# Optimization experiments

Hardware: AMD Instinct MI355X
Metric: run time of the kernel (lower is better)

## Reference

```python
import jax, jax.numpy as jnp
import numpy as np
import math

DIM = 768
K1 = 112
K2 = 224


def setup_inputs() -> dict:
    key = jax.random.key(0)
    ks = jax.random.split(key, 10)
    B, N, D = 256, 196, DIM
    inp = {
        "rgb_patches": jax.random.normal(ks[0], (B, N, D), jnp.float32),
        "nir_patches": jax.random.normal(ks[1], (B, N, D), jnp.float32),
        "tir_patches": jax.random.normal(ks[2], (B, N, D), jnp.float32),
        "rgb_global": jax.random.normal(ks[3], (B, D), jnp.float32),
        "nir_global": jax.random.normal(ks[4], (B, D), jnp.float32),
        "tir_global": jax.random.normal(ks[5], (B, D), jnp.float32),
        # nn.Linear params (W_v is defined in the torch module but never used in forward)
        "Wq": jax.random.normal(ks[6], (D, D), jnp.float32) / math.sqrt(D),
        "bq": jnp.zeros((D,), jnp.float32),
        "Wk": jax.random.normal(ks[7], (D, D), jnp.float32) / math.sqrt(D),
        "bk": jnp.zeros((D,), jnp.float32),
    }
    return inp


def _scatter_ones(idx, B, n):
    # idx: [B, K] in [0, n] where value n means "drop" (scattered into pad slot)
    rows = jnp.arange(B)[:, None]
    m = jnp.zeros((B, n + 1), jnp.float32).at[rows, idx].set(1.0)
    return m[:, :n]


def _intra_mask(patches, g, scale):
    # scores over own-modality patches
    B, N, _ = patches.shape
    scores = jax.nn.softmax(jnp.einsum('bd,bnd->bn', g, patches) * scale, axis=1)
    _, idx = jax.lax.top_k(scores, min(K1, N))
    return _scatter_ones(idx, B, N)


def _split_scatter(idx, B, n_a, n_b):
    # idx indexes concat([a (len n_a), b (len n_b)]); route to two masks
    idx_a = jnp.where(idx < n_a, idx, n_a)          # pad slot n_a when not a
    idx_b = jnp.where(idx >= n_a, idx - n_a, n_b)   # pad slot n_b when not b
    return _scatter_ones(idx_a, B, n_a), _scatter_ones(idx_b, B, n_b)


def reference(rgb_patches, nir_patches, tir_patches, rgb_global, nir_global, tir_global, Wq, bq, Wk, bk):
    B, n_rgb, D = rgb_patches.shape
    n_nir = nir_patches.shape[1]
    n_tir = tir_patches.shape[1]
    scale = 1.0 / math.sqrt(D)

    # ---- intra-modal selection ----
    rgb_mask_i = _intra_mask(rgb_patches, rgb_global, scale)
    nir_mask_i = _intra_mask(nir_patches, nir_global, scale)
    tir_mask_i = _intra_mask(tir_patches, tir_global, scale)

    # ---- inter-modal selection ----
    queries = jnp.stack([rgb_global, nir_global, tir_global], axis=1)        # [B,3,D]
    keys = jnp.concatenate([rgb_patches, nir_patches, tir_patches], axis=1)  # [B,3N,D]
    q = queries @ Wq.T + bq
    k = keys @ Wk.T + bk
    scores = jax.nn.softmax(jnp.einsum('bqd,bnd->bqn', q, k) * scale, axis=2)

    rgb_scores = jnp.concatenate([scores[:, 0, n_rgb:n_rgb + n_nir], scores[:, 0, n_rgb + n_nir:]], axis=1)
    nir_scores = jnp.concatenate([scores[:, 1, :n_rgb], scores[:, 1, n_rgb + n_nir:]], axis=1)
    tir_scores = jnp.concatenate([scores[:, 2, :n_rgb], scores[:, 2, n_rgb:n_rgb + n_nir]], axis=1)

    _, rgb_idx = jax.lax.top_k(rgb_scores, min(K2, rgb_scores.shape[1]))
    _, nir_idx = jax.lax.top_k(nir_scores, min(K2, nir_scores.shape[1]))
    _, tir_idx = jax.lax.top_k(tir_scores, min(K2, tir_scores.shape[1]))

    # rgb query selects among [nir, tir]; nir query among [rgb, tir]; tir query among [rgb, nir]
    nir_m1, tir_m1 = _split_scatter(rgb_idx, B, n_nir, n_tir)
    rgb_m1, tir_m2 = _split_scatter(nir_idx, B, n_rgb, n_tir)
    rgb_m2, nir_m2 = _split_scatter(tir_idx, B, n_rgb, n_nir)

    rgb_mask_c = jnp.maximum(rgb_m1, rgb_m2)
    nir_mask_c = jnp.maximum(nir_m1, nir_m2)
    tir_mask_c = jnp.maximum(tir_m1, tir_m2)

    # ---- union of masks, apply ----
    rgb_mask = (rgb_mask_c + rgb_mask_i > 0).astype(rgb_patches.dtype)[..., None]
    nir_mask = (nir_mask_c + nir_mask_i > 0).astype(nir_patches.dtype)[..., None]
    tir_mask = (tir_mask_c + tir_mask_i > 0).astype(tir_patches.dtype)[..., None]

    return (rgb_patches * rgb_mask, nir_patches * nir_mask, tir_patches * tir_mask)
```

## Files before the change

### kernel.cpp

```cpp
#include <hip/hip_runtime.h>

#define DD   768
#define BB   256
#define NN   196
#define KK1  112
#define KK2  224
#define RTOT (BB*3)
#define CAND (2*NN)


__global__ __launch_bounds__(256) void gemm_q(
    const float* __restrict__ g0, const float* __restrict__ g1,
    const float* __restrict__ g2, const float* __restrict__ Wq,
    const float* __restrict__ bq, double* __restrict__ Qh)
{
    __shared__ float As[32][33];
    __shared__ float Ws[32][33];
    const int t  = threadIdx.x;
    const int tx = t & 15, ty = t >> 4;
    const int i0 = blockIdx.y * 32, j0 = blockIdx.x * 32;
    double a00 = 0, a01 = 0, a10 = 0, a11 = 0;
    for (int kk = 0; kk < DD; kk += 32) {
        for (int s = 0; s < 4; ++s) {
            int idx = t + s * 256;
            int r = idx >> 5, c = idx & 31;
            int row = i0 + r;
            int b = row / 3, q = row - b * 3;
            const float* gp = (q == 0) ? g0 : (q == 1) ? g1 : g2;
            As[r][c] = gp[b * DD + kk + c];
            Ws[r][c] = Wq[(j0 + r) * DD + kk + c];
        }
        __syncthreads();
        for (int k = 0; k < 32; ++k) {
            double x0 = (double)As[ty][k],      x1 = (double)As[ty + 16][k];
            double y0 = (double)Ws[tx][k],      y1 = (double)Ws[tx + 16][k];
            a00 += x0 * y0; a01 += x0 * y1; a10 += x1 * y0; a11 += x1 * y1;
        }
        __syncthreads();
    }
    Qh[(i0 + ty) * DD + j0 + tx]           = a00 + (double)bq[j0 + tx];
    Qh[(i0 + ty) * DD + j0 + tx + 16]      = a01 + (double)bq[j0 + tx + 16];
    Qh[(i0 + ty + 16) * DD + j0 + tx]      = a10 + (double)bq[j0 + tx];
    Qh[(i0 + ty + 16) * DD + j0 + tx + 16] = a11 + (double)bq[j0 + tx + 16];
}

__global__ __launch_bounds__(256) void gemm_t(
    const double* __restrict__ Qh, const float* __restrict__ Wk,
    double* __restrict__ Td)
{
    __shared__ double As[32][33];
    __shared__ float  Ws[32][33];
    const int t  = threadIdx.x;
    const int tx = t & 15, ty = t >> 4;
    const int i0 = blockIdx.y * 32, j0 = blockIdx.x * 32;
    double a00 = 0, a01 = 0, a10 = 0, a11 = 0;
    for (int kk = 0; kk < DD; kk += 32) {
        for (int s = 0; s < 4; ++s) {
            int idx = t + s * 256;
            int r = idx >> 5, c = idx & 31;
            As[r][c] = Qh[(i0 + r) * DD + kk + c];
            Ws[r][c] = Wk[(kk + r) * DD + j0 + c];
        }
        __syncthreads();
        for (int k = 0; k < 32; ++k) {
            double x0 = As[ty][k],            x1 = As[ty + 16][k];
            double y0 = (double)Ws[k][tx],    y1 = (double)Ws[k][tx + 16];
            a00 += x0 * y0; a01 += x0 * y1; a10 += x1 * y0; a11 += x1 * y1;
        }
        __syncthreads();
    }
    Td[(i0 + ty) * DD + j0 + tx]           = a00;
    Td[(i0 + ty) * DD + j0 + tx + 16]      = a01;
    Td[(i0 + ty + 16) * DD + j0 + tx]      = a10;
    Td[(i0 + ty + 16) * DD + j0 + tx + 16] = a11;
}

__global__ __launch_bounds__(256) void score_kernel(
    const float* __restrict__ p0, const float* __restrict__ p1,
    const float* __restrict__ p2, const float* __restrict__ g0,
    const float* __restrict__ g1, const float* __restrict__ g2,
    const double* __restrict__ Td, double* __restrict__ Lintra,
    double* __restrict__ Linter)
{
    const int bm = blockIdx.x;
    const int b = bm / 3, m = bm - b * 3;
    __shared__ double gd[DD], Ta[DD], Tb[DD];

    const float* gp = (m == 0) ? g0 : (m == 1) ? g1 : g2;
    const float* pp = (m == 0) ? p0 : (m == 1) ? p1 : p2;
    const int qa = (m == 0) ? 1 : 0;
    const int qb = (m == 2) ? 1 : 2;
    const int slota = m - (m > qa ? 1 : 0);
    const int slotb = m - (m > qb ? 1 : 0);

    for (int d = threadIdx.x; d < DD; d += 256) {
        gd[d] = (double)gp[b * DD + d];
        Ta[d] = Td[(b * 3 + qa) * DD + d];
        Tb[d] = Td[(b * 3 + qb) * DD + d];
    }
    __syncthreads();

    const int wave = threadIdx.x >> 6, lane = threadIdx.x & 63;
    for (int n = wave; n < NN; n += 4) {
        const float4* row = (const float4*)(pp + (size_t)(b * NN + n) * DD);
        double s0 = 0, s1 = 0, s2 = 0;
        for (int c = lane; c < DD / 4; c += 64) {
            float4 v = row[c];
            int d = c * 4;
            s0 += gd[d] * (double)v.x + gd[d + 1] * (double)v.y
                + gd[d + 2] * (double)v.z + gd[d + 3] * (double)v.w;
            s1 += Ta[d] * (double)v.x + Ta[d + 1] * (double)v.y
                + Ta[d + 2] * (double)v.z + Ta[d + 3] * (double)v.w;
            s2 += Tb[d] * (double)v.x + Tb[d + 1] * (double)v.y
                + Tb[d + 2] * (double)v.z + Tb[d + 3] * (double)v.w;
        }
        for (int off = 32; off > 0; off >>= 1) {
            s0 += __shfl_down(s0, off);
            s1 += __shfl_down(s1, off);
            s2 += __shfl_down(s2, off);
        }
        if (lane == 0) {
            Lintra[bm * NN + n]                          = s0;
            Linter[(b * 3 + qa) * CAND + slota * NN + n] = s1;
            Linter[(b * 3 + qb) * CAND + slotb * NN + n] = s2;
        }
    }
}

__global__ __launch_bounds__(256) void rank_intra(
    const double* __restrict__ Lintra, unsigned char* __restrict__ mask)
{
    const int bm = blockIdx.x;
    const int b = bm / 3, m = bm - b * 3;
    __shared__ double L[NN];
    for (int i = threadIdx.x; i < NN; i += 256) L[i] = Lintra[bm * NN + i];
    __syncthreads();
    const int t = threadIdx.x;
    if (t < NN) {
        double v = L[t];
        int rank = 0;
        for (int j = 0; j < NN; ++j) {
            double u = L[j];
            rank += (u > v) || (u == v && j < t);
        }
        if (rank < KK1) mask[m * (BB * NN) + b * NN + t] = 1;
    }
}

__global__ __launch_bounds__(256) void rank_inter(
    const double* __restrict__ Linter, unsigned char* __restrict__ mask)
{
    const int bq = blockIdx.x;
    const int b = bq / 3, q = bq - b * 3;
    __shared__ double L[CAND];
    for (int i = threadIdx.x; i < CAND; i += 256) L[i] = Linter[bq * CAND + i];
    __syncthreads();
    const int ma = (q == 0) ? 1 : 0;
    const int mb = (q == 2) ? 1 : 2;
    for (int t = threadIdx.x; t < CAND; t += 256) {
        double v = L[t];
        int rank = 0;
        for (int j = 0; j < CAND; ++j) {
            double u = L[j];
            rank += (u > v) || (u == v && j < t);
        }
        if (rank < KK2) {
            int mm  = (t < NN) ? ma : mb;
            int tok = (t < NN) ? t : t - NN;
            mask[mm * (BB * NN) + b * NN + tok] = 1;
        }
    }
}

__global__ __launch_bounds__(192) void apply_mask(
    const float* __restrict__ p0, const float* __restrict__ p1,
    const float* __restrict__ p2, const unsigned char* __restrict__ mask,
    float* __restrict__ out)
{
    const int row  = blockIdx.x;
    const int m    = row / (BB * NN);
    const int lrow = row - m * (BB * NN);
    const float* pp = (m == 0) ? p0 : (m == 1) ? p1 : p2;
    const float4* src = (const float4*)(pp + (size_t)lrow * DD);
    float4*       dst = (float4*)(out + (size_t)row * DD);
    if (mask[row]) {
        dst[threadIdx.x] = src[threadIdx.x];
    } else {
        float4 z; z.x = 0.f; z.y = 0.f; z.z = 0.f; z.w = 0.f;
        dst[threadIdx.x] = z;
    }
}

extern "C" void kernel_launch(void* const* d_in, const int* in_sizes, int n_in,
                              void* d_out, int out_size, void* d_ws, size_t ws_size,
                              hipStream_t stream) {
    const float* p0 = (const float*)d_in[0];
    const float* p1 = (const float*)d_in[1];
    const float* p2 = (const float*)d_in[2];
    const float* g0 = (const float*)d_in[3];
    const float* g1 = (const float*)d_in[4];
    const float* g2 = (const float*)d_in[5];
    const float* Wq = (const float*)d_in[6];
    const float* bq = (const float*)d_in[7];
    const float* Wk = (const float*)d_in[8];

    char* ws = (char*)d_ws;
    double*        Qh     = (double*)(ws);
    double*        Td     = (double*)(ws + 4718592);
    double*        Lintra = (double*)(ws + 9437184);
    double*        Linter = (double*)(ws + 10641408);
    unsigned char* mask   = (unsigned char*)(ws + 13049856);

    hipMemsetAsync(mask, 0, 3 * BB * NN, stream);

    dim3 ggrid(DD / 32, RTOT / 32);
    gemm_q<<<ggrid, 256, 0, stream>>>(g0, g1, g2, Wq, bq, Qh);
    gemm_t<<<ggrid, 256, 0, stream>>>(Qh, Wk, Td);
    score_kernel<<<RTOT, 256, 0, stream>>>(p0, p1, p2, g0, g1, g2, Td, Lintra, Linter);
    rank_intra<<<RTOT, 256, 0, stream>>>(Lintra, mask);
    rank_inter<<<RTOT, 256, 0, stream>>>(Linter, mask);
    apply_mask<<<3 * BB * NN, 192, 0, stream>>>(p0, p1, p2, mask, (float*)d_out);
}
```

Baseline: 1.007 ms.

## Fuse scoring, ranking and masking into one per-batch kernel writing output in-pass

```diff
diff --git a/kernel.cpp b/kernel.cpp
--- a/kernel.cpp
+++ b/kernel.cpp
@@ -7,6 +7,8 @@
 #define KK2  224
 #define RTOT (BB*3)
 #define CAND (2*NN)
+
+typedef float vfloat4 __attribute__((ext_vector_type(4)));
 
 
 __global__ __launch_bounds__(256) void gemm_q(
@@ -75,44 +77,52 @@
     Td[(i0 + ty + 16) * DD + j0 + tx + 16] = a11;
 }
 
-__global__ __launch_bounds__(256) void score_kernel(
+__global__ __launch_bounds__(1024) void fused_score_rank_apply(
     const float* __restrict__ p0, const float* __restrict__ p1,
     const float* __restrict__ p2, const float* __restrict__ g0,
     const float* __restrict__ g1, const float* __restrict__ g2,
-    const double* __restrict__ Td, double* __restrict__ Lintra,
-    double* __restrict__ Linter)
+    const double* __restrict__ Td, float* __restrict__ out)
 {
-    const int bm = blockIdx.x;
-    const int b = bm / 3, m = bm - b * 3;
-    __shared__ double gd[DD], Ta[DD], Tb[DD];
-
-    const float* gp = (m == 0) ? g0 : (m == 1) ? g1 : g2;
-    const float* pp = (m == 0) ? p0 : (m == 1) ? p1 : p2;
-    const int qa = (m == 0) ? 1 : 0;
-    const int qb = (m == 2) ? 1 : 2;
-    const int slota = m - (m > qa ? 1 : 0);
-    const int slotb = m - (m > qb ? 1 : 0);
-
-    for (int d = threadIdx.x; d < DD; d += 256) {
-        gd[d] = (double)gp[b * DD + d];
-        Ta[d] = Td[(b * 3 + qa) * DD + d];
-        Tb[d] = Td[(b * 3 + qb) * DD + d];
-    }
+    const int b = blockIdx.x;
+    __shared__ float  Gf[3][DD];
+    __shared__ double Tq[3][DD];
+    __shared__ double Li[3][NN];
+    __shared__ double Le[3][CAND];
+    __shared__ unsigned char msk[3][NN];
+
+    for (int d = threadIdx.x; d < DD; d += 1024) {
+        Gf[0][d] = g0[b * DD + d];
+        Gf[1][d] = g1[b * DD + d];
+        Gf[2][d] = g2[b * DD + d];
+        Tq[0][d] = Td[(b * 3 + 0) * DD + d];
+        Tq[1][d] = Td[(b * 3 + 1) * DD + d];
+        Tq[2][d] = Td[(b * 3 + 2) * DD + d];
+    }
+    if (threadIdx.x < 3 * NN) (&msk[0][0])[threadIdx.x] = 0;
     __syncthreads();
 
     const int wave = threadIdx.x >> 6, lane = threadIdx.x & 63;
-    for (int n = wave; n < NN; n += 4) {
-        const float4* row = (const float4*)(pp + (size_t)(b * NN + n) * DD);
+
+    for (int r = wave; r < 3 * NN; r += 16) {
+        const int m = r / NN, n = r - m * NN;
+        const float* pp = (m == 0) ? p0 : (m == 1) ? p1 : p2;
+        const vfloat4* row = (const vfloat4*)(pp + (size_t)(b * NN + n) * DD);
+        vfloat4* orow = (vfloat4*)(out + ((size_t)m * (BB * NN) + b * NN + n) * (size_t)DD);
+        const int qa = (m == 0) ? 1 : 0;
+        const int qb = (m == 2) ? 1 : 2;
+        const int slota = m - (m > qa ? 1 : 0);
+        const int slotb = m - (m > qb ? 1 : 0);
         double s0 = 0, s1 = 0, s2 = 0;
         for (int c = lane; c < DD / 4; c += 64) {
-            float4 v = row[c];
-            int d = c * 4;
-            s0 += gd[d] * (double)v.x + gd[d + 1] * (double)v.y
-                + gd[d + 2] * (double)v.z + gd[d + 3] * (double)v.w;
-            s1 += Ta[d] * (double)v.x + Ta[d + 1] * (double)v.y
-                + Ta[d + 2] * (double)v.z + Ta[d + 3] * (double)v.w;
-            s2 += Tb[d] * (double)v.x + Tb[d + 1] * (double)v.y
-                + Tb[d + 2] * (double)v.z + Tb[d + 3] * (double)v.w;
+            vfloat4 v = row[c];
+            __builtin_nontemporal_store(v, &orow[c]);
+            const int d = c * 4;
+            s0 += (double)Gf[m][d]     * (double)v[0] + (double)Gf[m][d + 1] * (double)v[1]
+                + (double)Gf[m][d + 2] * (double)v[2] + (double)Gf[m][d + 3] * (double)v[3];
+            s1 += Tq[qa][d]     * (double)v[0] + Tq[qa][d + 1] * (double)v[1]
+                + Tq[qa][d + 2] * (double)v[2] + Tq[qa][d + 3] * (double)v[3];
+            s2 += Tq[qb][d]     * (double)v[0] + Tq[qb][d + 1] * (double)v[1]
+                + Tq[qb][d + 2] * (double)v[2] + Tq[qb][d + 3] * (double)v[3];
         }
         for (int off = 32; off > 0; off >>= 1) {
             s0 += __shfl_down(s0, off);
@@ -120,74 +130,49 @@
             s2 += __shfl_down(s2, off);
         }
         if (lane == 0) {
-            Lintra[bm * NN + n]                          = s0;
-            Linter[(b * 3 + qa) * CAND + slota * NN + n] = s1;
-            Linter[(b * 3 + qb) * CAND + slotb * NN + n] = s2;
-        }
-    }
-}
-
-__global__ __launch_bounds__(256) void rank_intra(
-    const double* __restrict__ Lintra, unsigned char* __restrict__ mask)
-{
-    const int bm = blockIdx.x;
-    const int b = bm / 3, m = bm - b * 3;
-    __shared__ double L[NN];
-    for (int i = threadIdx.x; i < NN; i += 256) L[i] = Lintra[bm * NN + i];
+            Li[m][n] = s0;
+            Le[qa][slota * NN + n] = s1;
+            Le[qb][slotb * NN + n] = s2;
+        }
+    }
     __syncthreads();
-    const int t = threadIdx.x;
-    if (t < NN) {
-        double v = L[t];
+
+    if (threadIdx.x < 3 * NN) {
+        const int m = threadIdx.x / NN, n = threadIdx.x - m * NN;
+        const double v = Li[m][n];
         int rank = 0;
         for (int j = 0; j < NN; ++j) {
-            double u = L[j];
-            rank += (u > v) || (u == v && j < t);
-        }
-        if (rank < KK1) mask[m * (BB * NN) + b * NN + t] = 1;
-    }
-}
-
-__global__ __launch_bounds__(256) void rank_inter(
-    const double* __restrict__ Linter, unsigned char* __restrict__ mask)
-{
-    const int bq = blockIdx.x;
-    const int b = bq / 3, q = bq - b * 3;
-    __shared__ double L[CAND];
-    for (int i = threadIdx.x; i < CAND; i += 256) L[i] = Linter[bq * CAND + i];
-    __syncthreads();
-    const int ma = (q == 0) ? 1 : 0;
-    const int mb = (q == 2) ? 1 : 2;
-    for (int t = threadIdx.x; t < CAND; t += 256) {
-        double v = L[t];
+            double u = Li[m][j];
+            rank += (u > v) || (u == v && j < n);
+        }
+        if (rank < KK1) msk[m][n] = 1;
+    }
+    for (int t = threadIdx.x; t < 3 * CAND; t += 1024) {
+        const int q = t / CAND, c = t - q * CAND;
+        const double v = Le[q][c];
         int rank = 0;
         for (int j = 0; j < CAND; ++j) {
-            double u = L[j];
-            rank += (u > v) || (u == v && j < t);
+            double u = Le[q][j];
+            rank += (u > v) || (u == v && j < c);
         }
         if (rank < KK2) {
-            int mm  = (t < NN) ? ma : mb;
-            int tok = (t < NN) ? t : t - NN;
-            mask[mm * (BB * NN) + b * NN + tok] = 1;
-        }
-    }
-}
-
-__global__ __launch_bounds__(192) void apply_mask(
-    const float* __restrict__ p0, const float* __restrict__ p1,
-    const float* __restrict__ p2, const unsigned char* __restrict__ mask,
-    float* __restrict__ out)
-{
-    const int row  = blockIdx.x;
-    const int m    = row / (BB * NN);
-    const int lrow = row - m * (BB * NN);
-    const float* pp = (m == 0) ? p0 : (m == 1) ? p1 : p2;
-    const float4* src = (const float4*)(pp + (size_t)lrow * DD);
-    float4*       dst = (float4*)(out + (size_t)row * DD);
-    if (mask[row]) {
-        dst[threadIdx.x] = src[threadIdx.x];
-    } else {
-        float4 z; z.x = 0.f; z.y = 0.f; z.z = 0.f; z.w = 0.f;
-        dst[threadIdx.x] = z;
+            const int ma = (q == 0) ? 1 : 0;
+            const int mb = (q == 2) ? 1 : 2;
+            const int mm  = (c < NN) ? ma : mb;
+            const int tok = (c < NN) ? c : c - NN;
+            msk[mm][tok] = 1;
+        }
+    }
+    __syncthreads();
+
+    for (int r = wave; r < 3 * NN; r += 16) {
+        const int m = r / NN, n = r - m * NN;
+        if (!msk[m][n]) {
+            vfloat4* orow = (vfloat4*)(out + ((size_t)m * (BB * NN) + b * NN + n) * (size_t)DD);
+            const vfloat4 z = {0.f, 0.f, 0.f, 0.f};
+            for (int c = lane; c < DD / 4; c += 64)
+                __builtin_nontemporal_store(z, &orow[c]);
+        }
     }
 }
 
@@ -205,19 +190,11 @@
     const float* Wk = (const float*)d_in[8];
 
     char* ws = (char*)d_ws;
-    double*        Qh     = (double*)(ws);
-    double*        Td     = (double*)(ws + 4718592);
-    double*        Lintra = (double*)(ws + 9437184);
-    double*        Linter = (double*)(ws + 10641408);
-    unsigned char* mask   = (unsigned char*)(ws + 13049856);
-
-    hipMemsetAsync(mask, 0, 3 * BB * NN, stream);
+    double* Qh = (double*)(ws);
+    double* Td = (double*)(ws + 4718592);
 
     dim3 ggrid(DD / 32, RTOT / 32);
     gemm_q<<<ggrid, 256, 0, stream>>>(g0, g1, g2, Wq, bq, Qh);
     gemm_t<<<ggrid, 256, 0, stream>>>(Qh, Wk, Td);
-    score_kernel<<<RTOT, 256, 0, stream>>>(p0, p1, p2, g0, g1, g2, Td, Lintra, Linter);
-    rank_intra<<<RTOT, 256, 0, stream>>>(Lintra, mask);
-    rank_inter<<<RTOT, 256, 0, stream>>>(Linter, mask);
-    apply_mask<<<3 * BB * NN, 192, 0, stream>>>(p0, p1, p2, mask, (float*)d_out);
-}
+    fused_score_rank_apply<<<BB, 1024, 0, stream>>>(p0, p1, p2, g0, g1, g2, Td, (float*)d_out);
+}
```

Measured after the change: 921.8 us. -8.5%, faster.
